# Performance work log

Measured on AMD Instinct MI355X. Metric: run time of the kernel, lower is better.

## Reference

```python
import jax, jax.numpy as jnp
import numpy as np


def setup_inputs() -> dict:
    key = jax.random.key(0)
    k1, k2 = jax.random.split(key)
    E, H, N = 3200000, 8, 100000
    logits = jax.random.normal(k1, (E, H, 1), dtype=jnp.float32)
    dst = jax.random.randint(k2, (E,), 0, N, dtype=jnp.int32)
    return {"logits": logits, "dst": dst, "num_nodes": N}


def reference(logits, dst, num_nodes):
    # scatter-max of edge logits into destination nodes: [N, H, 1]
    max_logits = jax.ops.segment_max(logits, dst, num_segments=num_nodes)
    # nodes with no incoming edges get -inf from segment_max; harmless since
    # no edge gathers from them, but sanitize normalizer path anyway.
    # exp(z_ij - max_i): [E, H, 1]
    scores = jnp.exp(logits - max_logits[dst])
    # scatter-sum of unnormalized scores per destination node: [N, H, 1]
    normalizer = jax.ops.segment_sum(scores, dst, num_segments=num_nodes)
    return scores, normalizer
```

## Files before the change

### kernel.cpp

```cpp
#include <hip/hip_runtime.h>


#define NPB_SHIFT 7
#define NPB 128
#define NBMAX 1024
#define CAP_B 5120
#define EPB 8192
#define RCACHE 16

__global__ void esb_zero_kernel(int* __restrict__ bcursor, int nb) {
    int i = blockIdx.x * blockDim.x + threadIdx.x;
    if (i < nb) bcursor[i] = 0;
}

__launch_bounds__(256)
__global__ void esb_bin_kernel(const int* __restrict__ dst,
                               int* __restrict__ bcursor,
                               unsigned int* __restrict__ entries,
                               int NB, int E) {
    __shared__ int hist[NBMAX];
    __shared__ int hbase[NBMAX];
    __shared__ int lcur[NBMAX];
    const int tid = threadIdx.x;
    const int base = blockIdx.x * EPB;

    for (int b = tid; b < NB; b += 256) hist[b] = 0;
    __syncthreads();

#pragma unroll
    for (int i = 0; i < EPB / 256; ++i) {
        int e = base + i * 256 + tid;
        if (e < E) {
            int b = dst[e] >> NPB_SHIFT;
            atomicAdd(&hist[b], 1);
        }
    }
    __syncthreads();

    for (int b = tid; b < NB; b += 256) {
        int c = hist[b];
        hbase[b] = c ? atomicAdd(&bcursor[b], c) : 0;
        lcur[b] = 0;
    }
    __syncthreads();

#pragma unroll
    for (int i = 0; i < EPB / 256; ++i) {
        int e = base + i * 256 + tid;
        if (e < E) {
            int d = dst[e];
            int b = d >> NPB_SHIFT;
            int p = atomicAdd(&lcur[b], 1);
            int idx = hbase[b] + p;
            if (idx < CAP_B)
                entries[(size_t)b * CAP_B + idx] =
                    ((unsigned int)(d & (NPB - 1)) << 22) | (unsigned int)e;
        }
    }
}

__launch_bounds__(512)
__global__ void esb_reduce_kernel(const float* __restrict__ logits,
                                  const int* __restrict__ bcursor,
                                  const unsigned int* __restrict__ entries,
                                  float* __restrict__ maxtab,
                                  float* __restrict__ norm,
                                  int N, int E) {
    __shared__ int counts[NPB];
    __shared__ int offs[NPB];
    __shared__ int lcur2[NPB];
    __shared__ int idlist[CAP_B];

    const int tid = threadIdx.x;
    const int b = blockIdx.x;
    const int node_base = b << NPB_SHIFT;
    const int nlocal = min(NPB, N - node_base);
    int cnt_b = bcursor[b];
    if (cnt_b > CAP_B) cnt_b = CAP_B;
    const unsigned int* ent = entries + (size_t)b * CAP_B;

    if (tid < NPB) counts[tid] = 0;
    __syncthreads();

    for (int i = tid; i < cnt_b; i += 512)
        atomicAdd(&counts[ent[i] >> 22], 1);
    __syncthreads();

    if (tid < 64) {
        int l = tid;
        int a0 = counts[2 * l], a1 = counts[2 * l + 1];
        int s = a0 + a1;
        int pref = s;
        for (int off = 1; off < 64; off <<= 1) {
            int t = __shfl_up(pref, off, 64);
            if (l >= off) pref += t;
        }
        pref -= s;
        offs[2 * l] = pref;
        offs[2 * l + 1] = pref + a0;
        lcur2[2 * l] = 0;
        lcur2[2 * l + 1] = 0;
    }
    __syncthreads();

    for (int i = tid; i < cnt_b; i += 512) {
        unsigned int en = ent[i];
        int ld = en >> 22;
        int p = atomicAdd(&lcur2[ld], 1);
        idlist[offs[ld] + p] = (int)(en & 0x3FFFFFu);
    }
    __syncthreads();

    const int wave = tid >> 6;
    const int lane = tid & 63;
    const int h = lane & 7;
    const int g = lane >> 3;
    const float NINF = __int_as_float(0xFF800000);

    for (int ld = wave; ld < nlocal; ld += 8) {
        int node = node_base + ld;
        int cnt = counts[ld];
        int ib = offs[ld];
        float m = NINF;
        float acc = 0.0f;

        if (cnt <= 8 * RCACHE) {
            float vals[RCACHE];
#pragma unroll
            for (int i = 0; i < RCACHE; ++i) {
                if (i * 8 >= cnt) break;
                int j = g + i * 8;
                bool ok = j < cnt;
                int eid = ok ? idlist[ib + j] : 0;
                float v = ok ? logits[(size_t)eid * 8 + h] : NINF;
                vals[i] = v;
                m = fmaxf(m, v);
            }
            m = fmaxf(m, __shfl_xor(m, 8, 64));
            m = fmaxf(m, __shfl_xor(m, 16, 64));
            m = fmaxf(m, __shfl_xor(m, 32, 64));
#pragma unroll
            for (int i = 0; i < RCACHE; ++i) {
                if (i * 8 >= cnt) break;
                if (g + i * 8 < cnt) acc += __expf(vals[i] - m);
            }
        } else {
            for (int j = g; j < cnt; j += 8)
                m = fmaxf(m, logits[(size_t)idlist[ib + j] * 8 + h]);
            m = fmaxf(m, __shfl_xor(m, 8, 64));
            m = fmaxf(m, __shfl_xor(m, 16, 64));
            m = fmaxf(m, __shfl_xor(m, 32, 64));
            for (int j = g; j < cnt; j += 8)
                acc += __expf(logits[(size_t)idlist[ib + j] * 8 + h] - m);
        }
        acc += __shfl_xor(acc, 8, 64);
        acc += __shfl_xor(acc, 16, 64);
        acc += __shfl_xor(acc, 32, 64);
        if (g == 0) norm[(size_t)node * 8 + h] = acc;
        if (g == 1) maxtab[(size_t)node * 8 + h] = m;
    }
}

__launch_bounds__(256)
__global__ void esb_score_kernel(const float* __restrict__ logits,
                                 const int* __restrict__ dst,
                                 const float* __restrict__ maxtab,
                                 float* __restrict__ scores, int E) {
    int e = blockIdx.x * blockDim.x + threadIdx.x;
    if (e >= E) return;
    int d = dst[e];
    const float4* lp = (const float4*)(logits + (size_t)e * 8);
    float4 a = lp[0];
    float4 bb = lp[1];
    const float4* mp = (const float4*)(maxtab + (size_t)d * 8);
    float4 m0 = mp[0];
    float4 m1 = mp[1];
    float4 s0, s1;
    s0.x = __expf(a.x - m0.x);
    s0.y = __expf(a.y - m0.y);
    s0.z = __expf(a.z - m0.z);
    s0.w = __expf(a.w - m0.w);
    s1.x = __expf(bb.x - m1.x);
    s1.y = __expf(bb.y - m1.y);
    s1.z = __expf(bb.z - m1.z);
    s1.w = __expf(bb.w - m1.w);
    float4* sp = (float4*)(scores + (size_t)e * 8);
    sp[0] = s0;
    sp[1] = s1;
}


__device__ __forceinline__ void atomicMaxFloat(float* addr, float value) {
    if (value >= 0.0f)
        atomicMax((int*)addr, __float_as_int(value));
    else
        atomicMin((unsigned int*)addr, __float_as_uint(value));
}

__global__ void es_init_kernel(unsigned int* __restrict__ maxws,
                               float* __restrict__ norm, int nh) {
    int i = blockIdx.x * blockDim.x + threadIdx.x;
    if (i < nh) {
        maxws[i] = 0xFF800000u;
        norm[i] = 0.0f;
    }
}

__global__ void es_max_gen_kernel(const float* __restrict__ logits,
                                  const int* __restrict__ dst,
                                  float* __restrict__ maxws,
                                  int total, int H) {
    int i = blockIdx.x * blockDim.x + threadIdx.x;
    if (i >= total) return;
    int e = i / H;
    int h = i - e * H;
    atomicMaxFloat(maxws + (size_t)dst[e] * H + h, logits[i]);
}

__global__ void es_score_gen_kernel(const float* __restrict__ logits,
                                    const int* __restrict__ dst,
                                    const float* __restrict__ maxws,
                                    float* __restrict__ scores,
                                    float* __restrict__ norm,
                                    int total, int H) {
    int i = blockIdx.x * blockDim.x + threadIdx.x;
    if (i >= total) return;
    int e = i / H;
    int h = i - e * H;
    size_t idx = (size_t)dst[e] * H + h;
    float s = __expf(logits[i] - maxws[idx]);
    scores[i] = s;
    atomicAdd(norm + idx, s);
}

extern "C" void kernel_launch(void* const* d_in, const int* in_sizes, int n_in,
                              void* d_out, int out_size, void* d_ws, size_t ws_size,
                              hipStream_t stream) {
    const float* logits = (const float*)d_in[0];
    const int* dst = (const int*)d_in[1];
    const int EH = in_sizes[0];
    const int E = in_sizes[1];
    const int H = EH / E;
    const int NH = out_size - EH;

    float* scores = (float*)d_out;
    float* norm = (float*)d_out + (size_t)EH;

    const int threads = 256;
    const int N = (H > 0) ? NH / H : 0;
    const int NB = (N + NPB - 1) >> NPB_SHIFT;

    const size_t need = ((size_t)NBMAX + (size_t)NB * CAP_B + (size_t)NH) * 4;

    if (H == 8 && N > 0 && NB <= NBMAX && E < (1 << 22) && ws_size >= need) {
        int* bcursor = (int*)d_ws;
        unsigned int* entries = (unsigned int*)d_ws + NBMAX;
        float* maxtab = (float*)((unsigned int*)d_ws + NBMAX + (size_t)NB * CAP_B);

        hipLaunchKernelGGL(esb_zero_kernel,
                           dim3((NB + threads - 1) / threads), dim3(threads), 0, stream,
                           bcursor, NB);

        hipLaunchKernelGGL(esb_bin_kernel,
                           dim3((E + EPB - 1) / EPB), dim3(threads), 0, stream,
                           dst, bcursor, entries, NB, E);

        hipLaunchKernelGGL(esb_reduce_kernel,
                           dim3(NB), dim3(512), 0, stream,
                           logits, bcursor, entries, maxtab, norm, N, E);

        hipLaunchKernelGGL(esb_score_kernel,
                           dim3((E + threads - 1) / threads), dim3(threads), 0, stream,
                           logits, dst, maxtab, scores, E);
    } else {
        float* maxws = (float*)d_ws;
        hipLaunchKernelGGL(es_init_kernel,
                           dim3((NH + threads - 1) / threads), dim3(threads), 0, stream,
                           (unsigned int*)maxws, norm, NH);
        int blocks = (EH + threads - 1) / threads;
        hipLaunchKernelGGL(es_max_gen_kernel, dim3(blocks), dim3(threads), 0, stream,
                           logits, dst, maxws, EH, H);
        hipLaunchKernelGGL(es_score_gen_kernel, dim3(blocks), dim3(threads), 0, stream,
                           logits, dst, maxws, scores, norm, EH, H);
    }
}
```

Baseline: 167.5 us.

## Copy logits into per-bin value buffers during binning to avoid random gathers

The binning kernel now writes each edge's 8 head logits, plus a one-byte local node id, into a per-bucket staging buffer instead of packing edge ids. The reduce kernel then reads values from its own contiguous bucket region through 16-bit positions held in LDS, rather than gathering logits from random edge ids. This is meant to turn scattered reads in the reduce into reads that stay local to one bucket. In exchange it adds roughly twice the logits size in extra global traffic and needs a much larger workspace; if the workspace is too small, execution falls back to the old path.

```diff
diff --git a/kernel.cpp b/kernel.cpp
--- a/kernel.cpp
+++ b/kernel.cpp
@@ -4,6 +4,7 @@
 #define NPB_SHIFT 7
 #define NPB 128
 #define NBMAX 1024
+#define CAP_V 4864
 #define CAP_B 5120
 #define EPB 8192
 #define RCACHE 16
@@ -13,11 +14,14 @@
     if (i < nb) bcursor[i] = 0;
 }
 
+
 __launch_bounds__(256)
-__global__ void esb_bin_kernel(const int* __restrict__ dst,
-                               int* __restrict__ bcursor,
-                               unsigned int* __restrict__ entries,
-                               int NB, int E) {
+__global__ void esbv_bin_kernel(const int* __restrict__ dst,
+                                const float* __restrict__ logits,
+                                int* __restrict__ bcursor,
+                                unsigned char* __restrict__ eld,
+                                float* __restrict__ eval,
+                                int NB, int E) {
     __shared__ int hist[NBMAX];
     __shared__ int hbase[NBMAX];
     __shared__ int lcur[NBMAX];
@@ -30,10 +34,7 @@
 #pragma unroll
     for (int i = 0; i < EPB / 256; ++i) {
         int e = base + i * 256 + tid;
-        if (e < E) {
-            int b = dst[e] >> NPB_SHIFT;
-            atomicAdd(&hist[b], 1);
-        }
+        if (e < E) atomicAdd(&hist[dst[e] >> NPB_SHIFT], 1);
     }
     __syncthreads();
 
@@ -52,38 +53,46 @@
             int b = d >> NPB_SHIFT;
             int p = atomicAdd(&lcur[b], 1);
             int idx = hbase[b] + p;
-            if (idx < CAP_B)
-                entries[(size_t)b * CAP_B + idx] =
-                    ((unsigned int)(d & (NPB - 1)) << 22) | (unsigned int)e;
+            if (idx < CAP_V) {
+                size_t g = (size_t)b * CAP_V + idx;
+                eld[g] = (unsigned char)(d & (NPB - 1));
+                const float4* lp = (const float4*)(logits + (size_t)e * 8);
+                float4* vp = (float4*)(eval + g * 8);
+                float4 v0 = lp[0];
+                float4 v1 = lp[1];
+                vp[0] = v0;
+                vp[1] = v1;
+            }
         }
     }
 }
 
 __launch_bounds__(512)
-__global__ void esb_reduce_kernel(const float* __restrict__ logits,
-                                  const int* __restrict__ bcursor,
-                                  const unsigned int* __restrict__ entries,
-                                  float* __restrict__ maxtab,
-                                  float* __restrict__ norm,
-                                  int N, int E) {
+__global__ void esbv_reduce_kernel(const int* __restrict__ bcursor,
+                                   const unsigned char* __restrict__ eld,
+                                   const float* __restrict__ eval,
+                                   float* __restrict__ maxtab,
+                                   float* __restrict__ norm,
+                                   int N) {
     __shared__ int counts[NPB];
     __shared__ int offs[NPB];
     __shared__ int lcur2[NPB];
-    __shared__ int idlist[CAP_B];
+    __shared__ unsigned short poslist[CAP_V];
 
     const int tid = threadIdx.x;
     const int b = blockIdx.x;
     const int node_base = b << NPB_SHIFT;
     const int nlocal = min(NPB, N - node_base);
     int cnt_b = bcursor[b];
-    if (cnt_b > CAP_B) cnt_b = CAP_B;
-    const unsigned int* ent = entries + (size_t)b * CAP_B;
+    if (cnt_b > CAP_V) cnt_b = CAP_V;
+    const unsigned char* ld_ = eld + (size_t)b * CAP_V;
+    const float* ev = eval + (size_t)b * CAP_V * 8;
 
     if (tid < NPB) counts[tid] = 0;
     __syncthreads();
 
     for (int i = tid; i < cnt_b; i += 512)
-        atomicAdd(&counts[ent[i] >> 22], 1);
+        atomicAdd(&counts[ld_[i]], 1);
     __syncthreads();
 
     if (tid < 64) {
@@ -104,10 +113,9 @@
     __syncthreads();
 
     for (int i = tid; i < cnt_b; i += 512) {
-        unsigned int en = ent[i];
-        int ld = en >> 22;
-        int p = atomicAdd(&lcur2[ld], 1);
-        idlist[offs[ld] + p] = (int)(en & 0x3FFFFFu);
+        int l = ld_[i];
+        int p = atomicAdd(&lcur2[l], 1);
+        poslist[offs[l] + p] = (unsigned short)i;
     }
     __syncthreads();
 
@@ -131,8 +139,8 @@
                 if (i * 8 >= cnt) break;
                 int j = g + i * 8;
                 bool ok = j < cnt;
-                int eid = ok ? idlist[ib + j] : 0;
-                float v = ok ? logits[(size_t)eid * 8 + h] : NINF;
+                int pos = ok ? (int)poslist[ib + j] : 0;
+                float v = ok ? ev[(size_t)pos * 8 + h] : NINF;
                 vals[i] = v;
                 m = fmaxf(m, v);
             }
@@ -146,12 +154,12 @@
             }
         } else {
             for (int j = g; j < cnt; j += 8)
-                m = fmaxf(m, logits[(size_t)idlist[ib + j] * 8 + h]);
+                m = fmaxf(m, ev[(size_t)poslist[ib + j] * 8 + h]);
             m = fmaxf(m, __shfl_xor(m, 8, 64));
             m = fmaxf(m, __shfl_xor(m, 16, 64));
             m = fmaxf(m, __shfl_xor(m, 32, 64));
             for (int j = g; j < cnt; j += 8)
-                acc += __expf(logits[(size_t)idlist[ib + j] * 8 + h] - m);
+                acc += __expf(ev[(size_t)poslist[ib + j] * 8 + h] - m);
         }
         acc += __shfl_xor(acc, 8, 64);
         acc += __shfl_xor(acc, 16, 64);
@@ -190,6 +198,145 @@
 }
 
 
+__launch_bounds__(256)
+__global__ void esb_bin_kernel(const int* __restrict__ dst,
+                               int* __restrict__ bcursor,
+                               unsigned int* __restrict__ entries,
+                               int NB, int E) {
+    __shared__ int hist[NBMAX];
+    __shared__ int hbase[NBMAX];
+    __shared__ int lcur[NBMAX];
+    const int tid = threadIdx.x;
+    const int base = blockIdx.x * EPB;
+
+    for (int b = tid; b < NB; b += 256) hist[b] = 0;
+    __syncthreads();
+#pragma unroll
+    for (int i = 0; i < EPB / 256; ++i) {
+        int e = base + i * 256 + tid;
+        if (e < E) atomicAdd(&hist[dst[e] >> NPB_SHIFT], 1);
+    }
+    __syncthreads();
+    for (int b = tid; b < NB; b += 256) {
+        int c = hist[b];
+        hbase[b] = c ? atomicAdd(&bcursor[b], c) : 0;
+        lcur[b] = 0;
+    }
+    __syncthreads();
+#pragma unroll
+    for (int i = 0; i < EPB / 256; ++i) {
+        int e = base + i * 256 + tid;
+        if (e < E) {
+            int d = dst[e];
+            int b = d >> NPB_SHIFT;
+            int p = atomicAdd(&lcur[b], 1);
+            int idx = hbase[b] + p;
+            if (idx < CAP_B)
+                entries[(size_t)b * CAP_B + idx] =
+                    ((unsigned int)(d & (NPB - 1)) << 22) | (unsigned int)e;
+        }
+    }
+}
+
+__launch_bounds__(512)
+__global__ void esb_reduce_kernel(const float* __restrict__ logits,
+                                  const int* __restrict__ bcursor,
+                                  const unsigned int* __restrict__ entries,
+                                  float* __restrict__ maxtab,
+                                  float* __restrict__ norm,
+                                  int N, int E) {
+    __shared__ int counts[NPB];
+    __shared__ int offs[NPB];
+    __shared__ int lcur2[NPB];
+    __shared__ int idlist[CAP_B];
+
+    const int tid = threadIdx.x;
+    const int b = blockIdx.x;
+    const int node_base = b << NPB_SHIFT;
+    const int nlocal = min(NPB, N - node_base);
+    int cnt_b = bcursor[b];
+    if (cnt_b > CAP_B) cnt_b = CAP_B;
+    const unsigned int* ent = entries + (size_t)b * CAP_B;
+
+    if (tid < NPB) counts[tid] = 0;
+    __syncthreads();
+    for (int i = tid; i < cnt_b; i += 512)
+        atomicAdd(&counts[ent[i] >> 22], 1);
+    __syncthreads();
+    if (tid < 64) {
+        int l = tid;
+        int a0 = counts[2 * l], a1 = counts[2 * l + 1];
+        int s = a0 + a1;
+        int pref = s;
+        for (int off = 1; off < 64; off <<= 1) {
+            int t = __shfl_up(pref, off, 64);
+            if (l >= off) pref += t;
+        }
+        pref -= s;
+        offs[2 * l] = pref;
+        offs[2 * l + 1] = pref + a0;
+        lcur2[2 * l] = 0;
+        lcur2[2 * l + 1] = 0;
+    }
+    __syncthreads();
+    for (int i = tid; i < cnt_b; i += 512) {
+        unsigned int en = ent[i];
+        int ld = en >> 22;
+        int p = atomicAdd(&lcur2[ld], 1);
+        idlist[offs[ld] + p] = (int)(en & 0x3FFFFFu);
+    }
+    __syncthreads();
+
+    const int wave = tid >> 6;
+    const int lane = tid & 63;
+    const int h = lane & 7;
+    const int g = lane >> 3;
+    const float NINF = __int_as_float(0xFF800000);
+
+    for (int ld = wave; ld < nlocal; ld += 8) {
+        int node = node_base + ld;
+        int cnt = counts[ld];
+        int ib = offs[ld];
+        float m = NINF;
+        float acc = 0.0f;
+        if (cnt <= 8 * RCACHE) {
+            float vals[RCACHE];
+#pragma unroll
+            for (int i = 0; i < RCACHE; ++i) {
+                if (i * 8 >= cnt) break;
+                int j = g + i * 8;
+                bool ok = j < cnt;
+                int eid = ok ? idlist[ib + j] : 0;
+                float v = ok ? logits[(size_t)eid * 8 + h] : NINF;
+                vals[i] = v;
+                m = fmaxf(m, v);
+            }
+            m = fmaxf(m, __shfl_xor(m, 8, 64));
+            m = fmaxf(m, __shfl_xor(m, 16, 64));
+            m = fmaxf(m, __shfl_xor(m, 32, 64));
+#pragma unroll
+            for (int i = 0; i < RCACHE; ++i) {
+                if (i * 8 >= cnt) break;
+                if (g + i * 8 < cnt) acc += __expf(vals[i] - m);
+            }
+        } else {
+            for (int j = g; j < cnt; j += 8)
+                m = fmaxf(m, logits[(size_t)idlist[ib + j] * 8 + h]);
+            m = fmaxf(m, __shfl_xor(m, 8, 64));
+            m = fmaxf(m, __shfl_xor(m, 16, 64));
+            m = fmaxf(m, __shfl_xor(m, 32, 64));
+            for (int j = g; j < cnt; j += 8)
+                acc += __expf(logits[(size_t)idlist[ib + j] * 8 + h] - m);
+        }
+        acc += __shfl_xor(acc, 8, 64);
+        acc += __shfl_xor(acc, 16, 64);
+        acc += __shfl_xor(acc, 32, 64);
+        if (g == 0) norm[(size_t)node * 8 + h] = acc;
+        if (g == 1) maxtab[(size_t)node * 8 + h] = m;
+    }
+}
+
+
 __device__ __forceinline__ void atomicMaxFloat(float* addr, float value) {
     if (value >= 0.0f)
         atomicMax((int*)addr, __float_as_int(value));
@@ -250,9 +397,29 @@
     const int N = (H > 0) ? NH / H : 0;
     const int NB = (N + NPB - 1) >> NPB_SHIFT;
 
-    const size_t need = ((size_t)NBMAX + (size_t)NB * CAP_B + (size_t)NH) * 4;
-
-    if (H == 8 && N > 0 && NB <= NBMAX && E < (1 << 22) && ws_size >= need) {
+    const size_t need_v = (size_t)NBMAX * 4 + (size_t)NB * CAP_V * 32 +
+                          (size_t)NB * CAP_V + (size_t)NH * 4;
+    const size_t need_i = (size_t)NBMAX * 4 + (size_t)NB * CAP_B * 4 + (size_t)NH * 4;
+
+    if (H == 8 && N > 0 && NB <= NBMAX && ws_size >= need_v) {
+        int* bcursor = (int*)d_ws;
+        float* eval = (float*)((char*)d_ws + (size_t)NBMAX * 4);
+        unsigned char* eld = (unsigned char*)(eval + (size_t)NB * CAP_V * 8);
+        float* maxtab = (float*)(eld + (size_t)NB * CAP_V);
+
+        hipLaunchKernelGGL(esb_zero_kernel,
+                           dim3((NB + threads - 1) / threads), dim3(threads), 0, stream,
+                           bcursor, NB);
+        hipLaunchKernelGGL(esbv_bin_kernel,
+                           dim3((E + EPB - 1) / EPB), dim3(threads), 0, stream,
+                           dst, logits, bcursor, eld, eval, NB, E);
+        hipLaunchKernelGGL(esbv_reduce_kernel,
+                           dim3(NB), dim3(512), 0, stream,
+                           bcursor, eld, eval, maxtab, norm, N);
+        hipLaunchKernelGGL(esb_score_kernel,
+                           dim3((E + threads - 1) / threads), dim3(threads), 0, stream,
+                           logits, dst, maxtab, scores, E);
+    } else if (H == 8 && N > 0 && NB <= NBMAX && E < (1 << 22) && ws_size >= need_i) {
         int* bcursor = (int*)d_ws;
         unsigned int* entries = (unsigned int*)d_ws + NBMAX;
         float* maxtab = (float*)((unsigned int*)d_ws + NBMAX + (size_t)NB * CAP_B);
@@ -260,15 +427,12 @@
         hipLaunchKernelGGL(esb_zero_kernel,
                            dim3((NB + threads - 1) / threads), dim3(threads), 0, stream,
                            bcursor, NB);
-
         hipLaunchKernelGGL(esb_bin_kernel,
                            dim3((E + EPB - 1) / EPB), dim3(threads), 0, stream,
                            dst, bcursor, entries, NB, E);
-
         hipLaunchKernelGGL(esb_reduce_kernel,
                            dim3(NB), dim3(512), 0, stream,
                            logits, bcursor, entries, maxtab, norm, N, E);
-
         hipLaunchKernelGGL(esb_score_kernel,
                            dim3((E + threads - 1) / threads), dim3(threads), 0, stream,
                            logits, dst, maxtab, scores, E);
```

Measured after the change: 275.1 us. 64.2% more time.

## Replace per-node counting-sort reduce with online-softmax shared-memory CAS accumulation

Applied to the files above, without the earlier changes.

The reduce kernel no longer sorts each bin's edges by destination node with a count, prefix-scan and scatter into an LDS id list. Instead each edge's logit is merged directly into a packed 64-bit (max, sum) cell in shared memory using an online-softmax update inside an atomicCAS loop. This removes two passes over the entries, the scan, and the two-pass max-then-exp per node. In exchange, CAS retries on popular nodes add contention, and the normalizer's summation order differs from a fixed two-pass reduction.

```diff
diff --git a/kernel.cpp b/kernel.cpp
--- a/kernel.cpp
+++ b/kernel.cpp
@@ -6,7 +6,6 @@
 #define NBMAX 1024
 #define CAP_B 5120
 #define EPB 8192
-#define RCACHE 16
 
 __global__ void esb_zero_kernel(int* __restrict__ bcursor, int nb) {
     int i = blockIdx.x * blockDim.x + threadIdx.x;
@@ -26,24 +25,18 @@
 
     for (int b = tid; b < NB; b += 256) hist[b] = 0;
     __syncthreads();
-
 #pragma unroll
     for (int i = 0; i < EPB / 256; ++i) {
         int e = base + i * 256 + tid;
-        if (e < E) {
-            int b = dst[e] >> NPB_SHIFT;
-            atomicAdd(&hist[b], 1);
-        }
-    }
-    __syncthreads();
-
+        if (e < E) atomicAdd(&hist[dst[e] >> NPB_SHIFT], 1);
+    }
+    __syncthreads();
     for (int b = tid; b < NB; b += 256) {
         int c = hist[b];
         hbase[b] = c ? atomicAdd(&bcursor[b], c) : 0;
         lcur[b] = 0;
     }
     __syncthreads();
-
 #pragma unroll
     for (int i = 0; i < EPB / 256; ++i) {
         int e = base + i * 256 + tid;
@@ -60,16 +53,13 @@
 }
 
 __launch_bounds__(512)
-__global__ void esb_reduce_kernel(const float* __restrict__ logits,
+__global__ void eso_reduce_kernel(const float* __restrict__ logits,
                                   const int* __restrict__ bcursor,
                                   const unsigned int* __restrict__ entries,
                                   float* __restrict__ maxtab,
                                   float* __restrict__ norm,
-                                  int N, int E) {
-    __shared__ int counts[NPB];
-    __shared__ int offs[NPB];
-    __shared__ int lcur2[NPB];
-    __shared__ int idlist[CAP_B];
+                                  int N) {
+    __shared__ unsigned long long state[NPB * 8];
 
     const int tid = threadIdx.x;
     const int b = blockIdx.x;
@@ -79,85 +69,45 @@
     if (cnt_b > CAP_B) cnt_b = CAP_B;
     const unsigned int* ent = entries + (size_t)b * CAP_B;
 
-    if (tid < NPB) counts[tid] = 0;
-    __syncthreads();
-
-    for (int i = tid; i < cnt_b; i += 512)
-        atomicAdd(&counts[ent[i] >> 22], 1);
-    __syncthreads();
-
-    if (tid < 64) {
-        int l = tid;
-        int a0 = counts[2 * l], a1 = counts[2 * l + 1];
-        int s = a0 + a1;
-        int pref = s;
-        for (int off = 1; off < 64; off <<= 1) {
-            int t = __shfl_up(pref, off, 64);
-            if (l >= off) pref += t;
+    const unsigned long long INIT = 0xFF800000ull;
+    for (int i = tid; i < NPB * 8; i += 512) state[i] = INIT;
+    __syncthreads();
+
+    const int h = tid & 7;
+    for (int p = (tid >> 3); p < cnt_b; p += 64) {
+        unsigned int en = ent[p];
+        int ld = (int)(en >> 22);
+        int eid = (int)(en & 0x3FFFFFu);
+        float v = logits[(size_t)eid * 8 + h];
+        unsigned long long* cell = &state[(ld << 3) + h];
+        unsigned long long old = *cell;
+        while (true) {
+            float m = __uint_as_float((unsigned int)(old & 0xFFFFFFFFull));
+            float s = __uint_as_float((unsigned int)(old >> 32));
+            float nm, ns;
+            if (v <= m) {
+                nm = m;
+                ns = s + __expf(v - m);
+            } else {
+                nm = v;
+                ns = s * __expf(m - v) + 1.0f;
+            }
+            unsigned long long nw =
+                ((unsigned long long)__float_as_uint(ns) << 32) |
+                (unsigned long long)__float_as_uint(nm);
+            unsigned long long prev = atomicCAS(cell, old, nw);
+            if (prev == old) break;
+            old = prev;
         }
-        pref -= s;
-        offs[2 * l] = pref;
-        offs[2 * l + 1] = pref + a0;
-        lcur2[2 * l] = 0;
-        lcur2[2 * l + 1] = 0;
-    }
-    __syncthreads();
-
-    for (int i = tid; i < cnt_b; i += 512) {
-        unsigned int en = ent[i];
-        int ld = en >> 22;
-        int p = atomicAdd(&lcur2[ld], 1);
-        idlist[offs[ld] + p] = (int)(en & 0x3FFFFFu);
-    }
-    __syncthreads();
-
-    const int wave = tid >> 6;
-    const int lane = tid & 63;
-    const int h = lane & 7;
-    const int g = lane >> 3;
-    const float NINF = __int_as_float(0xFF800000);
-
-    for (int ld = wave; ld < nlocal; ld += 8) {
-        int node = node_base + ld;
-        int cnt = counts[ld];
-        int ib = offs[ld];
-        float m = NINF;
-        float acc = 0.0f;
-
-        if (cnt <= 8 * RCACHE) {
-            float vals[RCACHE];
-#pragma unroll
-            for (int i = 0; i < RCACHE; ++i) {
-                if (i * 8 >= cnt) break;
-                int j = g + i * 8;
-                bool ok = j < cnt;
-                int eid = ok ? idlist[ib + j] : 0;
-                float v = ok ? logits[(size_t)eid * 8 + h] : NINF;
-                vals[i] = v;
-                m = fmaxf(m, v);
-            }
-            m = fmaxf(m, __shfl_xor(m, 8, 64));
-            m = fmaxf(m, __shfl_xor(m, 16, 64));
-            m = fmaxf(m, __shfl_xor(m, 32, 64));
-#pragma unroll
-            for (int i = 0; i < RCACHE; ++i) {
-                if (i * 8 >= cnt) break;
-                if (g + i * 8 < cnt) acc += __expf(vals[i] - m);
-            }
-        } else {
-            for (int j = g; j < cnt; j += 8)
-                m = fmaxf(m, logits[(size_t)idlist[ib + j] * 8 + h]);
-            m = fmaxf(m, __shfl_xor(m, 8, 64));
-            m = fmaxf(m, __shfl_xor(m, 16, 64));
-            m = fmaxf(m, __shfl_xor(m, 32, 64));
-            for (int j = g; j < cnt; j += 8)
-                acc += __expf(logits[(size_t)idlist[ib + j] * 8 + h] - m);
-        }
-        acc += __shfl_xor(acc, 8, 64);
-        acc += __shfl_xor(acc, 16, 64);
-        acc += __shfl_xor(acc, 32, 64);
-        if (g == 0) norm[(size_t)node * 8 + h] = acc;
-        if (g == 1) maxtab[(size_t)node * 8 + h] = m;
+    }
+    __syncthreads();
+
+    for (int i = tid; i < nlocal * 8; i += 512) {
+        unsigned long long st = state[i];
+        maxtab[((size_t)node_base << 3) + i] =
+            __uint_as_float((unsigned int)(st & 0xFFFFFFFFull));
+        norm[((size_t)node_base << 3) + i] =
+            __uint_as_float((unsigned int)(st >> 32));
     }
 }
 
@@ -250,7 +200,7 @@
     const int N = (H > 0) ? NH / H : 0;
     const int NB = (N + NPB - 1) >> NPB_SHIFT;
 
-    const size_t need = ((size_t)NBMAX + (size_t)NB * CAP_B + (size_t)NH) * 4;
+    const size_t need = (size_t)NBMAX * 4 + (size_t)NB * CAP_B * 4 + (size_t)NH * 4;
 
     if (H == 8 && N > 0 && NB <= NBMAX && E < (1 << 22) && ws_size >= need) {
         int* bcursor = (int*)d_ws;
@@ -260,15 +210,12 @@
         hipLaunchKernelGGL(esb_zero_kernel,
                            dim3((NB + threads - 1) / threads), dim3(threads), 0, stream,
                            bcursor, NB);
-
         hipLaunchKernelGGL(esb_bin_kernel,
                            dim3((E + EPB - 1) / EPB), dim3(threads), 0, stream,
                            dst, bcursor, entries, NB, E);
-
-        hipLaunchKernelGGL(esb_reduce_kernel,
+        hipLaunchKernelGGL(eso_reduce_kernel,
                            dim3(NB), dim3(512), 0, stream,
-                           logits, bcursor, entries, maxtab, norm, N, E);
-
+                           logits, bcursor, entries, maxtab, norm, N);
         hipLaunchKernelGGL(esb_score_kernel,
                            dim3((E + threads - 1) / threads), dim3(threads), 0, stream,
                            logits, dst, maxtab, scores, E);
```

Result: no change. 166.7 us (-0.5%).

## Vectorize bin and reduce kernels, cache dst in registers, stage outputs in LDS

Applied to the files above, without the earlier changes.

The bin kernel now uses 512 threads and loads dst as int4 into registers once, reusing them in both the histogram and scatter passes instead of reading dst twice. The reduce kernel moves to 1024 threads and reads entries as uint4. Its register-cache loop is fully unrolled without early break. Per-node max and sum results are staged in shared memory and written out coalesced. This trades higher register and LDS pressure, and possibly lower occupancy, for fewer global loads and better coalescing.

```diff
diff --git a/kernel.cpp b/kernel.cpp
--- a/kernel.cpp
+++ b/kernel.cpp
@@ -6,38 +6,57 @@
 #define NBMAX 1024
 #define CAP_B 5120
 #define EPB 8192
-#define RCACHE 16
+#define BT 512
+#define RT 1024
 
 __global__ void esb_zero_kernel(int* __restrict__ bcursor, int nb) {
     int i = blockIdx.x * blockDim.x + threadIdx.x;
     if (i < nb) bcursor[i] = 0;
 }
 
-__launch_bounds__(256)
-__global__ void esb_bin_kernel(const int* __restrict__ dst,
-                               int* __restrict__ bcursor,
-                               unsigned int* __restrict__ entries,
-                               int NB, int E) {
+__launch_bounds__(BT)
+__global__ void esb_bin2_kernel(const int* __restrict__ dst,
+                                int* __restrict__ bcursor,
+                                unsigned int* __restrict__ entries,
+                                int NB, int E) {
     __shared__ int hist[NBMAX];
     __shared__ int hbase[NBMAX];
     __shared__ int lcur[NBMAX];
     const int tid = threadIdx.x;
     const int base = blockIdx.x * EPB;
-
-    for (int b = tid; b < NB; b += 256) hist[b] = 0;
-    __syncthreads();
-
-#pragma unroll
-    for (int i = 0; i < EPB / 256; ++i) {
-        int e = base + i * 256 + tid;
-        if (e < E) {
-            int b = dst[e] >> NPB_SHIFT;
-            atomicAdd(&hist[b], 1);
-        }
-    }
-    __syncthreads();
-
-    for (int b = tid; b < NB; b += 256) {
+    const bool full = (base + EPB) <= E;
+
+    for (int b = tid; b < NB; b += BT) hist[b] = 0;
+    __syncthreads();
+
+    int4 dreg[4];
+    if (full) {
+        const int4* dp = (const int4*)(dst + base);
+#pragma unroll
+        for (int i = 0; i < 4; ++i) {
+            dreg[i] = dp[i * BT + tid];
+            atomicAdd(&hist[dreg[i].x >> NPB_SHIFT], 1);
+            atomicAdd(&hist[dreg[i].y >> NPB_SHIFT], 1);
+            atomicAdd(&hist[dreg[i].z >> NPB_SHIFT], 1);
+            atomicAdd(&hist[dreg[i].w >> NPB_SHIFT], 1);
+        }
+    } else {
+#pragma unroll
+        for (int i = 0; i < 4; ++i) {
+            int e0 = base + (i * BT + tid) * 4;
+            dreg[i].x = (e0 + 0 < E) ? dst[e0 + 0] : -1;
+            dreg[i].y = (e0 + 1 < E) ? dst[e0 + 1] : -1;
+            dreg[i].z = (e0 + 2 < E) ? dst[e0 + 2] : -1;
+            dreg[i].w = (e0 + 3 < E) ? dst[e0 + 3] : -1;
+            if (dreg[i].x >= 0) atomicAdd(&hist[dreg[i].x >> NPB_SHIFT], 1);
+            if (dreg[i].y >= 0) atomicAdd(&hist[dreg[i].y >> NPB_SHIFT], 1);
+            if (dreg[i].z >= 0) atomicAdd(&hist[dreg[i].z >> NPB_SHIFT], 1);
+            if (dreg[i].w >= 0) atomicAdd(&hist[dreg[i].w >> NPB_SHIFT], 1);
+        }
+    }
+    __syncthreads();
+
+    for (int b = tid; b < NB; b += BT) {
         int c = hist[b];
         hbase[b] = c ? atomicAdd(&bcursor[b], c) : 0;
         lcur[b] = 0;
@@ -45,31 +64,37 @@
     __syncthreads();
 
 #pragma unroll
-    for (int i = 0; i < EPB / 256; ++i) {
-        int e = base + i * 256 + tid;
-        if (e < E) {
-            int d = dst[e];
-            int b = d >> NPB_SHIFT;
-            int p = atomicAdd(&lcur[b], 1);
-            int idx = hbase[b] + p;
-            if (idx < CAP_B)
-                entries[(size_t)b * CAP_B + idx] =
-                    ((unsigned int)(d & (NPB - 1)) << 22) | (unsigned int)e;
-        }
-    }
-}
-
-__launch_bounds__(512)
-__global__ void esb_reduce_kernel(const float* __restrict__ logits,
-                                  const int* __restrict__ bcursor,
-                                  const unsigned int* __restrict__ entries,
-                                  float* __restrict__ maxtab,
-                                  float* __restrict__ norm,
-                                  int N, int E) {
+    for (int i = 0; i < 4; ++i) {
+        int e0 = base + (i * BT + tid) * 4;
+        int dv[4] = {dreg[i].x, dreg[i].y, dreg[i].z, dreg[i].w};
+#pragma unroll
+        for (int c = 0; c < 4; ++c) {
+            int d = dv[c];
+            if (d >= 0) {
+                int bk = d >> NPB_SHIFT;
+                int p = atomicAdd(&lcur[bk], 1);
+                int idx = hbase[bk] + p;
+                if (idx < CAP_B)
+                    entries[(size_t)bk * CAP_B + idx] =
+                        ((unsigned int)(d & (NPB - 1)) << 22) | (unsigned int)(e0 + c);
+            }
+        }
+    }
+}
+
+__launch_bounds__(RT)
+__global__ void eso3_reduce_kernel(const float* __restrict__ logits,
+                                   const int* __restrict__ bcursor,
+                                   const unsigned int* __restrict__ entries,
+                                   float* __restrict__ maxtab,
+                                   float* __restrict__ norm,
+                                   int N) {
     __shared__ int counts[NPB];
     __shared__ int offs[NPB];
     __shared__ int lcur2[NPB];
     __shared__ int idlist[CAP_B];
+    __shared__ float mres[NPB * 8];
+    __shared__ float sres[NPB * 8];
 
     const int tid = threadIdx.x;
     const int b = blockIdx.x;
@@ -82,7 +107,15 @@
     if (tid < NPB) counts[tid] = 0;
     __syncthreads();
 
-    for (int i = tid; i < cnt_b; i += 512)
+    const int main4 = cnt_b >> 2;
+    for (int i = tid; i < main4; i += RT) {
+        uint4 q = ((const uint4*)ent)[i];
+        atomicAdd(&counts[q.x >> 22], 1);
+        atomicAdd(&counts[q.y >> 22], 1);
+        atomicAdd(&counts[q.z >> 22], 1);
+        atomicAdd(&counts[q.w >> 22], 1);
+    }
+    for (int i = (main4 << 2) + tid; i < cnt_b; i += RT)
         atomicAdd(&counts[ent[i] >> 22], 1);
     __syncthreads();
 
@@ -103,11 +136,19 @@
     }
     __syncthreads();
 
-    for (int i = tid; i < cnt_b; i += 512) {
+    for (int i = tid; i < main4; i += RT) {
+        uint4 q = ((const uint4*)ent)[i];
+        int l, p;
+        l = (int)(q.x >> 22); p = atomicAdd(&lcur2[l], 1); idlist[offs[l] + p] = (int)(q.x & 0x3FFFFFu);
+        l = (int)(q.y >> 22); p = atomicAdd(&lcur2[l], 1); idlist[offs[l] + p] = (int)(q.y & 0x3FFFFFu);
+        l = (int)(q.z >> 22); p = atomicAdd(&lcur2[l], 1); idlist[offs[l] + p] = (int)(q.z & 0x3FFFFFu);
+        l = (int)(q.w >> 22); p = atomicAdd(&lcur2[l], 1); idlist[offs[l] + p] = (int)(q.w & 0x3FFFFFu);
+    }
+    for (int i = (main4 << 2) + tid; i < cnt_b; i += RT) {
         unsigned int en = ent[i];
-        int ld = en >> 22;
-        int p = atomicAdd(&lcur2[ld], 1);
-        idlist[offs[ld] + p] = (int)(en & 0x3FFFFFu);
+        int l = (int)(en >> 22);
+        int p = atomicAdd(&lcur2[l], 1);
+        idlist[offs[l] + p] = (int)(en & 0x3FFFFFu);
     }
     __syncthreads();
 
@@ -117,21 +158,19 @@
     const int g = lane >> 3;
     const float NINF = __int_as_float(0xFF800000);
 
-    for (int ld = wave; ld < nlocal; ld += 8) {
-        int node = node_base + ld;
+    for (int ld = wave; ld < nlocal; ld += 16) {
         int cnt = counts[ld];
         int ib = offs[ld];
         float m = NINF;
         float acc = 0.0f;
 
-        if (cnt <= 8 * RCACHE) {
-            float vals[RCACHE];
-#pragma unroll
-            for (int i = 0; i < RCACHE; ++i) {
-                if (i * 8 >= cnt) break;
+        if (cnt <= 8 * 16) {
+            float vals[16];
+#pragma unroll
+            for (int i = 0; i < 16; ++i) {
                 int j = g + i * 8;
                 bool ok = j < cnt;
-                int eid = ok ? idlist[ib + j] : 0;
+                int eid = idlist[ok ? (ib + j) : 0];
                 float v = ok ? logits[(size_t)eid * 8 + h] : NINF;
                 vals[i] = v;
                 m = fmaxf(m, v);
@@ -140,8 +179,7 @@
             m = fmaxf(m, __shfl_xor(m, 16, 64));
             m = fmaxf(m, __shfl_xor(m, 32, 64));
 #pragma unroll
-            for (int i = 0; i < RCACHE; ++i) {
-                if (i * 8 >= cnt) break;
+            for (int i = 0; i < 16; ++i) {
                 if (g + i * 8 < cnt) acc += __expf(vals[i] - m);
             }
         } else {
@@ -156,8 +194,16 @@
         acc += __shfl_xor(acc, 8, 64);
         acc += __shfl_xor(acc, 16, 64);
         acc += __shfl_xor(acc, 32, 64);
-        if (g == 0) norm[(size_t)node * 8 + h] = acc;
-        if (g == 1) maxtab[(size_t)node * 8 + h] = m;
+        if (g == 0) {
+            mres[ld * 8 + h] = m;
+            sres[ld * 8 + h] = acc;
+        }
+    }
+    __syncthreads();
+
+    for (int i = tid; i < nlocal * 8; i += RT) {
+        maxtab[((size_t)node_base << 3) + i] = mres[i];
+        norm[((size_t)node_base << 3) + i] = sres[i];
     }
 }
 
@@ -250,7 +296,7 @@
     const int N = (H > 0) ? NH / H : 0;
     const int NB = (N + NPB - 1) >> NPB_SHIFT;
 
-    const size_t need = ((size_t)NBMAX + (size_t)NB * CAP_B + (size_t)NH) * 4;
+    const size_t need = (size_t)NBMAX * 4 + (size_t)NB * CAP_B * 4 + (size_t)NH * 4;
 
     if (H == 8 && N > 0 && NB <= NBMAX && E < (1 << 22) && ws_size >= need) {
         int* bcursor = (int*)d_ws;
@@ -260,15 +306,12 @@
         hipLaunchKernelGGL(esb_zero_kernel,
                            dim3((NB + threads - 1) / threads), dim3(threads), 0, stream,
                            bcursor, NB);
-
-        hipLaunchKernelGGL(esb_bin_kernel,
-                           dim3((E + EPB - 1) / EPB), dim3(threads), 0, stream,
+        hipLaunchKernelGGL(esb_bin2_kernel,
+                           dim3((E + EPB - 1) / EPB), dim3(BT), 0, stream,
                            dst, bcursor, entries, NB, E);
-
-        hipLaunchKernelGGL(esb_reduce_kernel,
-                           dim3(NB), dim3(512), 0, stream,
-                           logits, bcursor, entries, maxtab, norm, N, E);
-
+        hipLaunchKernelGGL(eso3_reduce_kernel,
+                           dim3(NB), dim3(RT), 0, stream,
+                           logits, bcursor, entries, maxtab, norm, N);
         hipLaunchKernelGGL(esb_score_kernel,
                            dim3((E + threads - 1) / threads), dim3(threads), 0, stream,
                            logits, dst, maxtab, scores, E);
```

Result: faster. 157.8 us (-5.8%).
